# Performance work log

Hardware: AMD Instinct MI355X
Metric: run time of the kernel (lower is better)

## Reference

```python
import jax, jax.numpy as jnp
import numpy as np

EPS = 1e-5  # BatchNorm1d default eps
NUM_HEADS = 8


def repbn(x, alpha, gamma, beta, rm, rv):
    # eval-mode RepBN over the channel (last) dim: BN(running stats) + alpha * x
    bn = (x - rm) * (gamma / jnp.sqrt(rv + EPS)) + beta
    return bn + alpha * x


def _forward(x, W_qkv, b_qkv, W_proj, b_proj, W1, b1, W2, b2, sa_w, sa_b,
             alpha1, gamma1, beta1, rm1, rv1, alpha2, gamma2, beta2, rm2, rv2):
    B, C, H, W = x.shape
    N = H * W
    D = C // NUM_HEADS
    t = x.reshape(B, C, N).transpose(0, 2, 1)  # [B, N, C]
    # --- FlashAttention (manual MHSA) ---
    qkv = (t @ W_qkv + b_qkv).reshape(B, N, 3, NUM_HEADS, D)
    q = qkv[:, :, 0].transpose(0, 2, 1, 3)  # [B, h, N, D]
    k = qkv[:, :, 1].transpose(0, 2, 1, 3)
    v = qkv[:, :, 2].transpose(0, 2, 1, 3)
    attn = jax.nn.softmax(jnp.einsum('bhnd,bhmd->bhnm', q, k) * (D ** -0.5), axis=-1)
    o = jnp.einsum('bhnm,bhmd->bhnd', attn, v).transpose(0, 2, 1, 3).reshape(B, N, C)
    o = o @ W_proj + b_proj
    # residual + blended norm (eval -> RepBN)
    t = repbn(t + o, alpha1, gamma1, beta1, rm1, rv1)
    # --- FFN with SpatialSILU activation ---
    h = t @ W1 + b1  # [B, N, cm]
    # depthwise 1x1 conv over the batch dim (channels==B per original unsqueeze(0))
    wgt = sa_w[:, None, None] * h + sa_b[:, None, None]
    h = h * jax.nn.sigmoid(wgt * h)
    f = h @ W2 + b2
    t = repbn(t + f, alpha2, gamma2, beta2, rm2, rv2)
    return t.transpose(0, 2, 1).reshape(B, C, H, W)


def setup_inputs() -> dict:
    key = jax.random.key(0)
    ks = jax.random.split(key, 8)
    B, C, H, W = 256, 256, 14, 14
    cm = 2048
    s = 0.02
    f32 = jnp.float32
    return {
        'x': jax.random.normal(ks[0], (B, C, H, W), f32),
        'W_qkv': jax.random.normal(ks[1], (C, 3 * C), f32) * s,
        'b_qkv': jnp.zeros((3 * C,), f32),
        'W_proj': jax.random.normal(ks[2], (C, C), f32) * s,
        'b_proj': jnp.zeros((C,), f32),
        'W1': jax.random.normal(ks[3], (C, cm), f32) * s,
        'b1': jnp.zeros((cm,), f32),
        'W2': jax.random.normal(ks[4], (cm, C), f32) * s,
        'b2': jnp.zeros((C,), f32),
        'sa_w': jax.random.normal(ks[5], (B,), f32) * s,
        'sa_b': jnp.zeros((B,), f32),
        'alpha1': jnp.ones((), f32),
        'gamma1': jnp.ones((C,), f32),
        'beta1': jnp.zeros((C,), f32),
        'rm1': jax.random.normal(ks[6], (C,), f32) * 0.1,
        'rv1': jnp.ones((C,), f32),
        'alpha2': jnp.ones((), f32),
        'gamma2': jnp.ones((C,), f32),
        'beta2': jnp.zeros((C,), f32),
        'rm2': jax.random.normal(ks[7], (C,), f32) * 0.1,
        'rv2': jnp.ones((C,), f32),
    }


def reference(x, W_qkv, b_qkv, W_proj, b_proj, W1, b1, W2, b2, sa_w, sa_b,
              alpha1, gamma1, beta1, rm1, rv1, alpha2, gamma2, beta2, rm2, rv2):
    return _forward(x, W_qkv, b_qkv, W_proj, b_proj, W1, b1, W2, b2, sa_w, sa_b,
                    alpha1, gamma1, beta1, rm1, rv1, alpha2, gamma2, beta2, rm2, rv2)
```

## Files before the change

kernel.cpp:

```cpp
#include <hip/hip_runtime.h>

using u16 = unsigned short;

typedef __bf16 bf16x8 __attribute__((ext_vector_type(8)));
typedef u16    u16x8  __attribute__((ext_vector_type(8)));
typedef float  f32x4  __attribute__((ext_vector_type(4)));

__device__ __forceinline__ float b2f(u16 u) {
    union { unsigned int i; float f; } c; c.i = ((unsigned int)u) << 16; return c.f;
}
__device__ __forceinline__ u16 f2b(float f) {
    union { float f; unsigned int i; } c; c.f = f;
    unsigned int i = c.i;
    return (u16)((i + 0x7FFFu + ((i >> 16) & 1u)) >> 16);
}
__device__ __forceinline__ float u2f(unsigned int u) {
    union { unsigned int i; float f; } c; c.i = u; return c.f;
}

#define AS1 __attribute__((address_space(1)))
#define AS3 __attribute__((address_space(3)))
__device__ __forceinline__ void glds16(const u16* g, u16* l) {
    __builtin_amdgcn_global_load_lds((const AS1 void*)(const void*)g,
                                     (AS3 void*)(void*)l, 16, 0, 0);
}

__global__ void btrans_f2b(const float* __restrict__ in, u16* __restrict__ out, int R, int C) {
    __shared__ u16 tile[32][33];
    const int c0 = blockIdx.x * 32, r0 = blockIdx.y * 32;
    const size_t base = (size_t)blockIdx.z * R * C;
    const int tx = threadIdx.x, ty = threadIdx.y;
    #pragma unroll
    for (int i = ty; i < 32; i += 8) {
        int r = r0 + i, c = c0 + tx;
        tile[i][tx] = (r < R && c < C) ? f2b(in[base + (size_t)r * C + c]) : (u16)0;
    }
    __syncthreads();
    #pragma unroll
    for (int i = ty; i < 32; i += 8) {
        int c = c0 + i, r = r0 + tx;
        if (c < C && r < R) out[base + (size_t)c * R + r] = tile[tx][i];
    }
}

__global__ void btrans_b2f(const u16* __restrict__ in, float* __restrict__ out, int R, int C) {
    __shared__ u16 tile[32][33];
    const int c0 = blockIdx.x * 32, r0 = blockIdx.y * 32;
    const size_t base = (size_t)blockIdx.z * R * C;
    const int tx = threadIdx.x, ty = threadIdx.y;
    #pragma unroll
    for (int i = ty; i < 32; i += 8) {
        int r = r0 + i, c = c0 + tx;
        tile[i][tx] = (r < R && c < C) ? in[base + (size_t)r * C + c] : (u16)0;
    }
    __syncthreads();
    #pragma unroll
    for (int i = ty; i < 32; i += 8) {
        int c = c0 + i, r = r0 + tx;
        if (c < C && r < R) out[base + (size_t)c * R + r] = b2f(tile[tx][i]);
    }
}

template<int EPI>
__launch_bounds__(512, 4)
__global__ void gemm_bt(const u16* __restrict__ A, const u16* __restrict__ BT,
                        const float* __restrict__ bias, u16* __restrict__ C,
                        int M, int N, int K, int row0,
                        const u16* __restrict__ R0,
                        const float* __restrict__ g, const float* __restrict__ be,
                        const float* __restrict__ rmv, const float* __restrict__ rvv,
                        const float* __restrict__ alpha,
                        const float* __restrict__ saw, const float* __restrict__ sab) {
    __shared__ __align__(16) u16 SL[16384];
    const int tid  = threadIdx.x;
    const int wave = tid >> 6, lane = tid & 63;
    const int wm = wave >> 2, wn = wave & 3;
    const int quad = lane >> 4, l16 = lane & 15;

    const unsigned gx = gridDim.x;
    unsigned lin = blockIdx.y * gx + blockIdx.x;
    const unsigned nwg = gx * gridDim.y;
    const unsigned q8 = nwg >> 3, r8 = nwg & 7;
    const unsigned xcd = lin & 7, loc = lin >> 3;
    lin = (xcd < r8 ? xcd * (q8 + 1) : r8 * (q8 + 1) + (xcd - r8) * q8) + loc;
    const int m0 = (int)(lin / gx) * 128, n0 = (int)(lin % gx) * 128;

    const int srow = lane >> 2;
    const int scol = (((lane & 3) ^ ((srow >> 1) & 3)) * 8);
    const size_t aoff = (size_t)(m0 + wave * 16 + srow) * K + scol;
    const size_t boff = (size_t)(n0 + wave * 16 + srow) * K + scol;
    u16* aS = SL + wave * 512;
    u16* bS = SL + 8192 + wave * 512;

    const int cfrag = (quad ^ ((l16 >> 1) & 3)) * 8;

    f32x4 acc[4][2] = {};
    const int niter = K >> 5;

    auto stage = [&](int buf, size_t kn) {
        const int bo = buf * 4096;
        glds16(A  + aoff + kn, aS + bo);
        glds16(BT + boff + kn, bS + bo);
    };

    auto kstep = [&](int cur, int kt) {
        __syncthreads();
        if (kt + 1 < niter) stage(cur ^ 1, (size_t)(kt + 1) << 5);
        const u16* ab = SL + cur * 4096;
        const u16* bb = SL + 8192 + cur * 4096;
        bf16x8 af[4], bfr[2];
        #pragma unroll
        for (int i = 0; i < 4; i++)
            af[i] = *(const bf16x8*)&ab[(wm * 64 + i * 16 + l16) * 32 + cfrag];
        #pragma unroll
        for (int j = 0; j < 2; j++)
            bfr[j] = *(const bf16x8*)&bb[(wn * 32 + j * 16 + l16) * 32 + cfrag];
        #pragma unroll
        for (int i = 0; i < 4; i++)
            #pragma unroll
            for (int j = 0; j < 2; j++)
                acc[i][j] = __builtin_amdgcn_mfma_f32_16x16x32_bf16(af[i], bfr[j], acc[i][j], 0, 0, 0);
    };

    stage(0, 0);
    int kt = 0;
    for (; kt + 2 <= niter; kt += 2) { kstep(0, kt); kstep(1, kt + 1); }
    if (kt < niter) kstep(kt & 1, kt);

    __syncthreads();

    float alphav = 0.f;
    if (EPI == 1) alphav = alpha[0];

    if (EPI == 1) {
        #pragma unroll
        for (int c = tid; c < 2048; c += 512) {
            int row = c >> 4, colc = (c & 15) * 8;
            *(u16x8*)&SL[row * 128 + colc] =
                *(const u16x8*)&R0[(size_t)(m0 + row) * N + n0 + colc];
        }
        __syncthreads();
    }

    float biasv[2], k0v[2], k1v[2];
    #pragma unroll
    for (int j = 0; j < 2; j++) {
        const int col = n0 + wn * 32 + j * 16 + l16;
        biasv[j] = bias[col];
        if (EPI == 1) {
            float sc = g[col] * rsqrtf(rvv[col] + 1e-5f);
            k1v[j] = sc + alphav;
            k0v[j] = be[col] - rmv[col] * sc;
        }
    }

    const int dup = l16 & 1;
    const int pr  = l16 >> 1;
    u16* Crow = C + (size_t)(m0 + wm * 64 + quad * 4 + 2 * dup) * N
                  + (n0 + wn * 32 + pr * 2);

    #pragma unroll
    for (int i = 0; i < 4; i++) {
        #pragma unroll
        for (int j = 0; j < 2; j++) {
            float vv[4];
            #pragma unroll
            for (int r = 0; r < 4; r++) {
                float v = acc[i][j][r] + biasv[j];
                if (EPI == 1) {
                    const int rowL = wm * 64 + i * 16 + quad * 4 + r;
                    const int colp = wn * 32 + j * 16 + (l16 & ~1);
                    unsigned rd = *(const unsigned*)&SL[rowL * 128 + colp];
                    unsigned fb = dup ? (rd & 0xffff0000u) : (rd << 16);
                    float x = v + u2f(fb);
                    v = fmaf(x, k1v[j], k0v[j]);
                } else if (EPI == 2) {
                    const int row = row0 + m0 + wm * 64 + i * 16 + quad * 4 + r;
                    const int bidx = row / 196;
                    float w = fmaf(saw[bidx], v, sab[bidx]);
                    v = v / (1.f + __expf(-w * v));
                }
                vv[r] = v;
            }
            unsigned D[4];
            #pragma unroll
            for (int r = 0; r < 4; r++) {
                float o  = __shfl_xor(vv[r], 1, 64);
                float lo = dup ? o : vv[r];
                float hi = dup ? vv[r] : o;
                unsigned d;
                asm("v_cvt_pk_bf16_f32 %0, %1, %2" : "=v"(d) : "v"(lo), "v"(hi));
                D[r] = d;
            }
            unsigned s0 = dup ? D[2] : D[0];
            unsigned s1 = dup ? D[3] : D[1];
            u16* p = Crow + (size_t)i * 16 * N + j * 16;
            *(unsigned*)p       = s0;
            *(unsigned*)(p + N) = s1;
        }
    }
}

__launch_bounds__(256)
__global__ void attn_kernel(const u16* __restrict__ qkv, u16* __restrict__ o) {
    __shared__ __align__(16) u16 Kb[224 * 32];
    __shared__ __align__(16) u16 Vt[32 * 232];
    __shared__ __align__(16) u16 Pl[4][16 * 232];
    const int tid  = threadIdx.x;
    const int wave = tid >> 6, lane = tid & 63;
    const int quad = lane >> 4, l16 = lane & 15;
    const int b = blockIdx.x >> 3, h = blockIdx.x & 7;
    const u16* qg = qkv + (size_t)b * 196 * 768 + h * 32;
    const float scale = 0.17677669529663687f;

    for (int idx = tid; idx < 896; idx += 256) {
        int row = idx >> 2, dp = (idx & 3) * 8;
        u16x8 kv = {};
        if (row < 196) kv = *(const u16x8*)&qg[(size_t)row * 768 + 256 + dp];
        *(u16x8*)&Kb[row * 32 + dp] = kv;
    }
    for (int idx = tid; idx < 224 * 32; idx += 256) {
        int row = idx >> 5, d = idx & 31;
        Vt[d * 232 + row] = (row < 196) ? qg[(size_t)row * 768 + 512 + d] : (u16)0;
    }
    for (int c = lane; c < 16 * 24; c += 64) {
        int m = c / 24, cc = 208 + (c % 24);
        Pl[wave][m * 232 + cc] = 0;
    }
    __syncthreads();

    for (int t = wave; t < 13; t += 4) {
        const int m0 = t * 16;
        bf16x8 aq = {};
        const int qrow = m0 + l16;
        if (qrow < 196) aq = *(const bf16x8*)&qg[(size_t)qrow * 768 + quad * 8];

        f32x4 s[13];
        #pragma unroll
        for (int ct = 0; ct < 13; ct++) {
            bf16x8 bk = *(const bf16x8*)&Kb[(ct * 16 + l16) * 32 + quad * 8];
            s[ct] = __builtin_amdgcn_mfma_f32_16x16x32_bf16(aq, bk, (f32x4){0.f, 0.f, 0.f, 0.f}, 0, 0, 0);
        }
        if (l16 >= 4) {
            #pragma unroll
            for (int r = 0; r < 4; r++) s[12][r] = -1e30f;
        }
        float mx[4] = {-1e30f, -1e30f, -1e30f, -1e30f};
        #pragma unroll
        for (int ct = 0; ct < 13; ct++)
            #pragma unroll
            for (int r = 0; r < 4; r++) mx[r] = fmaxf(mx[r], s[ct][r]);
        #pragma unroll
        for (int off = 1; off < 16; off <<= 1)
            #pragma unroll
            for (int r = 0; r < 4; r++) mx[r] = fmaxf(mx[r], __shfl_xor(mx[r], off, 64));
        float sum[4] = {0.f, 0.f, 0.f, 0.f};
        #pragma unroll
        for (int ct = 0; ct < 13; ct++) {
            #pragma unroll
            for (int r = 0; r < 4; r++) {
                float p = __expf((s[ct][r] - mx[r]) * scale);
                sum[r] += p;
                Pl[wave][(quad * 4 + r) * 232 + ct * 16 + l16] = f2b(p);
            }
        }
        #pragma unroll
        for (int off = 1; off < 16; off <<= 1)
            #pragma unroll
            for (int r = 0; r < 4; r++) sum[r] += __shfl_xor(sum[r], off, 64);
        float inv[4];
        #pragma unroll
        for (int r = 0; r < 4; r++) inv[r] = 1.f / sum[r];

        #pragma unroll
        for (int nt = 0; nt < 2; nt++) {
            f32x4 ao = {0.f, 0.f, 0.f, 0.f};
            #pragma unroll
            for (int kc = 0; kc < 7; kc++) {
                bf16x8 ap = *(const bf16x8*)&Pl[wave][l16 * 232 + kc * 32 + quad * 8];
                bf16x8 bv = *(const bf16x8*)&Vt[(nt * 16 + l16) * 232 + kc * 32 + quad * 8];
                ao = __builtin_amdgcn_mfma_f32_16x16x32_bf16(ap, bv, ao, 0, 0, 0);
            }
            #pragma unroll
            for (int r = 0; r < 4; r++) {
                const int gm = m0 + quad * 4 + r;
                if (gm < 196)
                    o[((size_t)b * 196 + gm) * 256 + h * 32 + nt * 16 + l16] = f2b(ao[r] * inv[r]);
            }
        }
    }
}

extern "C" void kernel_launch(void* const* d_in, const int* in_sizes, int n_in,
                              void* d_out, int out_size, void* d_ws, size_t ws_size,
                              hipStream_t stream) {
    const float* x      = (const float*)d_in[0];
    const float* Wqkv   = (const float*)d_in[1];
    const float* bqkv   = (const float*)d_in[2];
    const float* Wproj  = (const float*)d_in[3];
    const float* bproj  = (const float*)d_in[4];
    const float* W1     = (const float*)d_in[5];
    const float* b1     = (const float*)d_in[6];
    const float* W2     = (const float*)d_in[7];
    const float* b2     = (const float*)d_in[8];
    const float* saw    = (const float*)d_in[9];
    const float* sab    = (const float*)d_in[10];
    const float* alpha1 = (const float*)d_in[11];
    const float* g1     = (const float*)d_in[12];
    const float* be1    = (const float*)d_in[13];
    const float* rm1    = (const float*)d_in[14];
    const float* rv1    = (const float*)d_in[15];
    const float* alpha2 = (const float*)d_in[16];
    const float* g2     = (const float*)d_in[17];
    const float* be2    = (const float*)d_in[18];
    const float* rm2    = (const float*)d_in[19];
    const float* rv2    = (const float*)d_in[20];

    const int B = 256, Cc = 256, Np = 196, CM = 2048;
    const int M = B * Np;

    auto al = [](size_t s) { return (s + 255) & ~(size_t)255; };
    char* ws = (char*)d_ws;
    const size_t o_t0  = 0;
    const size_t o_t1  = o_t0 + al((size_t)M * Cc * 2);
    const size_t o_wq  = o_t1 + al((size_t)M * Cc * 2);
    const size_t o_wp  = o_wq + al((size_t)768 * Cc * 2);
    const size_t o_w1  = o_wp + al((size_t)Cc * Cc * 2);
    const size_t o_w2  = o_w1 + al((size_t)Cc * CM * 2);
    const size_t o_scr = o_w2 + al((size_t)CM * Cc * 2);
    const size_t S = (ws_size > o_scr) ? ws_size - o_scr : 0;

    u16* t0     = (u16*)(ws + o_t0);
    u16* t1b    = (u16*)(ws + o_t1);
    u16* WqkvT  = (u16*)(ws + o_wq);
    u16* WprojT = (u16*)(ws + o_wp);
    u16* W1T    = (u16*)(ws + o_w1);
    u16* W2T    = (u16*)(ws + o_w2);
    u16* scr    = (u16*)(ws + o_scr);
    u16* t2     = t0;
    u16* obuf   = (u16*)d_out;
    float* out  = (float*)d_out;

    int nq = 1; while (nq < 8 && ((size_t)(M / nq) * 768 * 2) > S) nq *= 2;
    const int nf_opts[7] = {1, 2, 4, 8, 14, 28, 56};
    int nf = 56;
    for (int i = 0; i < 7; ++i) {
        if (((size_t)(M / nf_opts[i]) * CM * 2) <= S) { nf = nf_opts[i]; break; }
    }
    const int Mq = M / nq, Bq = B / nq;
    const int Mf = M / nf;

    dim3 tb(32, 8, 1);
    btrans_f2b<<<dim3((Np + 31) / 32, (Cc + 31) / 32, B), tb, 0, stream>>>(x, t0, Cc, Np);
    btrans_f2b<<<dim3(768 / 32, Cc / 32, 1), tb, 0, stream>>>(Wqkv,  WqkvT,  Cc, 768);
    btrans_f2b<<<dim3(Cc  / 32, Cc / 32, 1), tb, 0, stream>>>(Wproj, WprojT, Cc, Cc);
    btrans_f2b<<<dim3(CM  / 32, Cc / 32, 1), tb, 0, stream>>>(W1,    W1T,    Cc, CM);
    btrans_f2b<<<dim3(Cc  / 32, CM / 32, 1), tb, 0, stream>>>(W2,    W2T,    CM, Cc);

    for (int c = 0; c < nq; ++c) {
        gemm_bt<0><<<dim3(768 / 128, Mq / 128), 512, 0, stream>>>(
            t0 + (size_t)c * Mq * Cc, WqkvT, bqkv, scr, Mq, 768, Cc, 0,
            nullptr, nullptr, nullptr, nullptr, nullptr, nullptr, nullptr, nullptr);
        attn_kernel<<<dim3(Bq * 8), 256, 0, stream>>>(scr, obuf + (size_t)c * Mq * Cc);
    }

    gemm_bt<1><<<dim3(Cc / 128, M / 128), 512, 0, stream>>>(
        obuf, WprojT, bproj, t1b, M, Cc, Cc, 0,
        t0, g1, be1, rm1, rv1, alpha1, nullptr, nullptr);

    for (int c = 0; c < nf; ++c) {
        gemm_bt<2><<<dim3(CM / 128, Mf / 128), 512, 0, stream>>>(
            t1b + (size_t)c * Mf * Cc, W1T, b1, scr, Mf, CM, Cc, c * Mf,
            nullptr, nullptr, nullptr, nullptr, nullptr, nullptr, saw, sab);
        gemm_bt<1><<<dim3(Cc / 128, Mf / 128), 512, 0, stream>>>(
            scr, W2T, b2, t2 + (size_t)c * Mf * Cc, Mf, Cc, CM, 0,
            t1b + (size_t)c * Mf * Cc, g2, be2, rm2, rv2, alpha2, nullptr, nullptr);
    }

    btrans_b2f<<<dim3((Cc + 31) / 32, (Np + 31) / 32, B), tb, 0, stream>>>(t2, out, Np, Cc);
}
```

Before: 542.9 us.

## Deepen GEMM K-tile to 64, streamline epilogues, vectorize V transpose load

Measured after the change: 729.7 us. +34.4%, slower.

```diff
diff --git a/kernel.cpp b/kernel.cpp
--- a/kernel.cpp
+++ b/kernel.cpp
@@ -14,8 +14,10 @@
     unsigned int i = c.i;
     return (u16)((i + 0x7FFFu + ((i >> 16) & 1u)) >> 16);
 }
-__device__ __forceinline__ float u2f(unsigned int u) {
-    union { unsigned int i; float f; } c; c.i = u; return c.f;
+__device__ __forceinline__ unsigned cvtpk(float lo, float hi) {
+    unsigned d;
+    asm("v_cvt_pk_bf16_f32 %0, %1, %2" : "=v"(d) : "v"(lo), "v"(hi));
+    return d;
 }
 
 #define AS1 __attribute__((address_space(1)))
@@ -71,7 +73,7 @@
                         const float* __restrict__ rmv, const float* __restrict__ rvv,
                         const float* __restrict__ alpha,
                         const float* __restrict__ saw, const float* __restrict__ sab) {
-    __shared__ __align__(16) u16 SL[16384];
+    __shared__ __align__(16) u16 SL[32768];
     const int tid  = threadIdx.x;
     const int wave = tid >> 6, lane = tid & 63;
     const int wm = wave >> 2, wn = wave & 3;
@@ -89,37 +91,40 @@
     const int scol = (((lane & 3) ^ ((srow >> 1) & 3)) * 8);
     const size_t aoff = (size_t)(m0 + wave * 16 + srow) * K + scol;
     const size_t boff = (size_t)(n0 + wave * 16 + srow) * K + scol;
-    u16* aS = SL + wave * 512;
-    u16* bS = SL + 8192 + wave * 512;
 
     const int cfrag = (quad ^ ((l16 >> 1) & 3)) * 8;
 
     f32x4 acc[4][2] = {};
-    const int niter = K >> 5;
+    const int niter = K >> 6;
 
     auto stage = [&](int buf, size_t kn) {
-        const int bo = buf * 4096;
-        glds16(A  + aoff + kn, aS + bo);
-        glds16(BT + boff + kn, bS + bo);
+        #pragma unroll
+        for (int kc = 0; kc < 2; kc++) {
+            glds16(A  + aoff + kn + kc * 32, SL + buf * 8192 + kc * 4096 + wave * 512);
+            glds16(BT + boff + kn + kc * 32, SL + 16384 + buf * 8192 + kc * 4096 + wave * 512);
+        }
     };
 
     auto kstep = [&](int cur, int kt) {
         __syncthreads();
-        if (kt + 1 < niter) stage(cur ^ 1, (size_t)(kt + 1) << 5);
-        const u16* ab = SL + cur * 4096;
-        const u16* bb = SL + 8192 + cur * 4096;
-        bf16x8 af[4], bfr[2];
-        #pragma unroll
-        for (int i = 0; i < 4; i++)
-            af[i] = *(const bf16x8*)&ab[(wm * 64 + i * 16 + l16) * 32 + cfrag];
-        #pragma unroll
-        for (int j = 0; j < 2; j++)
-            bfr[j] = *(const bf16x8*)&bb[(wn * 32 + j * 16 + l16) * 32 + cfrag];
-        #pragma unroll
-        for (int i = 0; i < 4; i++)
+        if (kt + 1 < niter) stage(cur ^ 1, (size_t)(kt + 1) << 6);
+        const u16* ab = SL + cur * 8192;
+        const u16* bb = SL + 16384 + cur * 8192;
+        #pragma unroll
+        for (int kk = 0; kk < 2; kk++) {
+            bf16x8 af[4], bfr[2];
+            #pragma unroll
+            for (int i = 0; i < 4; i++)
+                af[i] = *(const bf16x8*)&ab[kk * 4096 + (wm * 64 + i * 16 + l16) * 32 + cfrag];
             #pragma unroll
             for (int j = 0; j < 2; j++)
-                acc[i][j] = __builtin_amdgcn_mfma_f32_16x16x32_bf16(af[i], bfr[j], acc[i][j], 0, 0, 0);
+                bfr[j] = *(const bf16x8*)&bb[kk * 4096 + (wn * 32 + j * 16 + l16) * 32 + cfrag];
+            #pragma unroll
+            for (int i = 0; i < 4; i++)
+                #pragma unroll
+                for (int j = 0; j < 2; j++)
+                    acc[i][j] = __builtin_amdgcn_mfma_f32_16x16x32_bf16(af[i], bfr[j], acc[i][j], 0, 0, 0);
+        }
     };
 
     stage(0, 0);
@@ -133,7 +138,6 @@
     if (EPI == 1) alphav = alpha[0];
 
     if (EPI == 1) {
-        #pragma unroll
         for (int c = tid; c < 2048; c += 512) {
             int row = c >> 4, colc = (c & 15) * 8;
             *(u16x8*)&SL[row * 128 + colc] =
@@ -142,61 +146,68 @@
         __syncthreads();
     }
 
-    float biasv[2], k0v[2], k1v[2];
-    #pragma unroll
-    for (int j = 0; j < 2; j++) {
-        const int col = n0 + wn * 32 + j * 16 + l16;
-        biasv[j] = bias[col];
-        if (EPI == 1) {
-            float sc = g[col] * rsqrtf(rvv[col] + 1e-5f);
-            k1v[j] = sc + alphav;
-            k0v[j] = be[col] - rmv[col] * sc;
-        }
-    }
-
+    float biasv[2], k0p[2][2], k1p[2][2];
     const int dup = l16 & 1;
     const int pr  = l16 >> 1;
+    #pragma unroll
+    for (int j = 0; j < 2; j++) {
+        biasv[j] = bias[n0 + wn * 32 + j * 16 + l16];
+        if (EPI == 1) {
+            #pragma unroll
+            for (int p = 0; p < 2; p++) {
+                const int col = n0 + wn * 32 + j * 16 + pr * 2 + p;
+                const float sc = g[col] * rsqrtf(rvv[col] + 1e-5f);
+                k1p[j][p] = sc + alphav;
+                k0p[j][p] = be[col] - rmv[col] * sc;
+            }
+        }
+    }
+
     u16* Crow = C + (size_t)(m0 + wm * 64 + quad * 4 + 2 * dup) * N
                   + (n0 + wn * 32 + pr * 2);
+    const int r0i = 2 * dup, r1i = r0i + 1;
 
     #pragma unroll
     for (int i = 0; i < 4; i++) {
+        float swv4[4], sbv4[4];
+        if (EPI == 2) {
+            #pragma unroll
+            for (int r = 0; r < 4; r++) {
+                const int row = row0 + m0 + wm * 64 + i * 16 + quad * 4 + r;
+                const int bidx = row / 196;
+                swv4[r] = saw[bidx]; sbv4[r] = sab[bidx];
+            }
+        }
         #pragma unroll
         for (int j = 0; j < 2; j++) {
             float vv[4];
             #pragma unroll
             for (int r = 0; r < 4; r++) {
                 float v = acc[i][j][r] + biasv[j];
-                if (EPI == 1) {
-                    const int rowL = wm * 64 + i * 16 + quad * 4 + r;
-                    const int colp = wn * 32 + j * 16 + (l16 & ~1);
-                    unsigned rd = *(const unsigned*)&SL[rowL * 128 + colp];
-                    unsigned fb = dup ? (rd & 0xffff0000u) : (rd << 16);
-                    float x = v + u2f(fb);
-                    v = fmaf(x, k1v[j], k0v[j]);
-                } else if (EPI == 2) {
-                    const int row = row0 + m0 + wm * 64 + i * 16 + quad * 4 + r;
-                    const int bidx = row / 196;
-                    float w = fmaf(saw[bidx], v, sab[bidx]);
+                if (EPI == 2) {
+                    float w = fmaf(swv4[r], v, sbv4[r]);
                     v = v / (1.f + __expf(-w * v));
                 }
                 vv[r] = v;
             }
-            unsigned D[4];
-            #pragma unroll
-            for (int r = 0; r < 4; r++) {
-                float o  = __shfl_xor(vv[r], 1, 64);
-                float lo = dup ? o : vv[r];
-                float hi = dup ? vv[r] : o;
-                unsigned d;
-                asm("v_cvt_pk_bf16_f32 %0, %1, %2" : "=v"(d) : "v"(lo), "v"(hi));
-                D[r] = d;
-            }
-            unsigned s0 = dup ? D[2] : D[0];
-            unsigned s1 = dup ? D[3] : D[1];
+            float ot[4];
+            #pragma unroll
+            for (int r = 0; r < 4; r++) ot[r] = __shfl_xor(vv[r], 1, 64);
+            float lo0 = dup ? ot[r0i] : vv[r0i], hi0 = dup ? vv[r0i] : ot[r0i];
+            float lo1 = dup ? ot[r1i] : vv[r1i], hi1 = dup ? vv[r1i] : ot[r1i];
+            if (EPI == 1) {
+                const int rowL = wm * 64 + i * 16 + quad * 4 + r0i;
+                const int colp = wn * 32 + j * 16 + pr * 2;
+                const unsigned rd0 = *(const unsigned*)&SL[rowL * 128 + colp];
+                const unsigned rd1 = *(const unsigned*)&SL[(rowL + 1) * 128 + colp];
+                lo0 = fmaf(lo0 + b2f((u16)(rd0 & 0xffff)), k1p[j][0], k0p[j][0]);
+                hi0 = fmaf(hi0 + b2f((u16)(rd0 >> 16)),    k1p[j][1], k0p[j][1]);
+                lo1 = fmaf(lo1 + b2f((u16)(rd1 & 0xffff)), k1p[j][0], k0p[j][0]);
+                hi1 = fmaf(hi1 + b2f((u16)(rd1 >> 16)),    k1p[j][1], k0p[j][1]);
+            }
             u16* p = Crow + (size_t)i * 16 * N + j * 16;
-            *(unsigned*)p       = s0;
-            *(unsigned*)(p + N) = s1;
+            *(unsigned*)p       = cvtpk(lo0, hi0);
+            *(unsigned*)(p + N) = cvtpk(lo1, hi1);
         }
     }
 }
@@ -219,9 +230,12 @@
         if (row < 196) kv = *(const u16x8*)&qg[(size_t)row * 768 + 256 + dp];
         *(u16x8*)&Kb[row * 32 + dp] = kv;
     }
-    for (int idx = tid; idx < 224 * 32; idx += 256) {
-        int row = idx >> 5, d = idx & 31;
-        Vt[d * 232 + row] = (row < 196) ? qg[(size_t)row * 768 + 512 + d] : (u16)0;
+    for (int idx = tid; idx < 896; idx += 256) {
+        int row = idx >> 2, dp = (idx & 3) * 8;
+        u16x8 vv = {};
+        if (row < 196) vv = *(const u16x8*)&qg[(size_t)row * 768 + 512 + dp];
+        #pragma unroll
+        for (int e = 0; e < 8; e++) Vt[(dp + e) * 232 + row] = vv[e];
     }
     for (int c = lane; c < 16 * 24; c += 64) {
         int m = c / 24, cc = 208 + (c % 24);
@@ -341,7 +355,7 @@
     u16* obuf   = (u16*)d_out;
     float* out  = (float*)d_out;
 
-    int nq = 1; while (nq < 8 && ((size_t)(M / nq) * 768 * 2) > S) nq *= 2;
+    int nq = 1; while (nq < 4 && ((size_t)(M / nq) * 768 * 2) > S) nq *= 2;
     const int nf_opts[7] = {1, 2, 4, 8, 14, 28, 56};
     int nf = 56;
     for (int i = 0; i < 7; ++i) {
```
